# Optimization experiments

Hardware: AMD Instinct MI355X
Metric: run time of the kernel (lower is better)

Reference implementation:

```python
import jax, jax.numpy as jnp
import numpy as np
from jax import lax

B, C, H, W = 4, 256, 64, 64
M = 8
CP = C // M  # 32 attention channels
KS = (3, 5, 7, 9)
EPS = 1e-5


def conv1x1(a, w, b):
    # a: [B,Ci,H,W], w: [Co,Ci], b: [Co]
    return jnp.einsum('bchw,oc->bohw', a, w) + b[None, :, None, None]


def _patches(a, k):
    # im2col with padding k//2, stride 1 (matches torch.nn.Unfold(k,1,k//2,1))
    pad = k // 2
    p = lax.conv_general_dilated_patches(a, (k, k), (1, 1), [(pad, pad), (pad, pad)])
    Bb, Cc = a.shape[0], a.shape[1]
    return p.reshape(Bb, Cc, k * k, a.shape[2], a.shape[3])  # [B,C',k^2,H,W]


def local_attn(km, qm, xm, k):
    # query is the center of each patch == qm itself (stride 1, pad k//2)
    kp = _patches(km, k)                                   # [B,C',k^2,H,W]
    scores = jnp.einsum('bckhw,bchw->bkhw', kp, qm)        # per-pixel k^2 logits
    attn = jax.nn.softmax(scores, axis=1)                  # softmax over window (dim=-2 in torch)
    xp = _patches(xm, k)                                   # [B,C',k^2,H,W]
    return jnp.einsum('bckhw,bkhw->bchw', xp, attn)        # [B,C',H,W]


def setup_inputs() -> dict:
    key = jax.random.key(0)
    ks = jax.random.split(key, 12)
    s_in = 1.0 / np.sqrt(C)
    s_out = 1.0 / np.sqrt(CP)
    return {
        'x': jax.random.normal(ks[0], (B, C, H, W), jnp.float32),
        'vessel': jax.random.uniform(ks[1], (B, 1, H, W), jnp.float32),
        'wk': jax.random.normal(ks[2], (CP, C), jnp.float32) * s_in,
        'bk': jnp.zeros((CP,), jnp.float32),
        'wq': jax.random.normal(ks[3], (CP, C), jnp.float32) * s_in,
        'bq': jnp.zeros((CP,), jnp.float32),
        'wx': jax.random.normal(ks[4], (CP, C), jnp.float32) * s_in,
        'bx': jnp.zeros((CP,), jnp.float32),
        'wf': jax.random.normal(ks[5], (C, CP), jnp.float32) * s_out,
        'bf': jnp.zeros((C,), jnp.float32),
        'gamma': jnp.ones((C,), jnp.float32),
        'beta': jnp.zeros((C,), jnp.float32),
    }


def reference(x, vessel, wk, bk, wq, bq, wx, bx, wf, bf, gamma, beta):
    km = conv1x1(x, wk, bk) * vessel   # key map masked by vessel
    qm = conv1x1(x, wq, bq)            # query map
    xm = conv1x1(x, wx, bx)            # value map
    pre = local_attn(km, qm, xm, KS[0])
    for k in KS[1:]:
        pre = pre + local_attn(km, qm, xm, k)
    y = conv1x1(pre, wf, bf)           # [B,C,H,W]
    # BatchNorm2d (training-mode batch stats)
    mean = y.mean(axis=(0, 2, 3), keepdims=True)
    var = y.var(axis=(0, 2, 3), keepdims=True)
    yn = (y - mean) * lax.rsqrt(var + EPS)
    return x + gamma[None, :, None, None] * yn + beta[None, :, None, None]
```

## Files before the change

### kernel.cpp

```cpp
#include <hip/hip_runtime.h>
#include <hip/hip_bf16.h>

typedef __hip_bfloat16 bf16;
typedef unsigned short u16;
typedef unsigned int u32;

typedef __bf16 bf16x8 __attribute__((ext_vector_type(8)));
typedef float f32x4 __attribute__((ext_vector_type(4)));

__device__ __forceinline__ float bf2f(bf16 v) { return __bfloat162float(v); }
__device__ __forceinline__ float us2f(u16 u) {
    union { u32 i; float f; } c; c.i = ((u32)u) << 16; return c.f;
}
__device__ __forceinline__ u16 f2u(float f) {
    union { bf16 b; u16 u; } c; c.b = __float2bfloat16(f); return c.u;
}

__global__ __launch_bounds__(256) void k_proj(
    const float* __restrict__ x, const float* __restrict__ vessel,
    const float* __restrict__ wk, const float* __restrict__ bk,
    const float* __restrict__ wq, const float* __restrict__ bq,
    const float* __restrict__ wx, const float* __restrict__ bx,
    bf16* __restrict__ km, bf16* __restrict__ qm, bf16* __restrict__ xm,
    float* __restrict__ partials)
{
    __shared__ u16 xs[64 * 264];
    __shared__ u16 wsh[48 * 264];
    const int tid = threadIdx.x;
    const int bid = blockIdx.x;
    const int nh = bid & 1;
    const int pt = bid >> 1;
    const int b  = pt >> 6;
    const int p0 = (pt & 63) * 64;

    if (bid < 64) {
#pragma unroll
        for (int i = 0; i < 5; ++i) {
            const int idx = tid + i * 256;
            if (idx < 1056) partials[bid * 1056 + idx] = 0.f;
        }
    }

#pragma unroll
    for (int i = 0; i < 16; ++i) {
        const int idx4 = tid + i * 256;
        const int ch = idx4 >> 4;
        const int px4 = (idx4 & 15) * 4;
        const float4 v = *(const float4*)&x[(b * 256 + ch) * 4096 + p0 + px4];
        xs[(px4 + 0) * 264 + ch] = f2u(v.x);
        xs[(px4 + 1) * 264 + ch] = f2u(v.y);
        xs[(px4 + 2) * 264 + ch] = f2u(v.z);
        xs[(px4 + 3) * 264 + ch] = f2u(v.w);
    }
#pragma unroll
    for (int i = 0; i < 12; ++i) {
        const int idx4 = tid + i * 256;
        const int o = idx4 >> 6;
        const int ch4 = (idx4 & 63) * 4;
        const int go = nh * 48 + o;
        const float* wp = (go < 32) ? wk : ((go < 64) ? wq : wx);
        const float4 v = *(const float4*)&wp[(go & 31) * 256 + ch4];
        wsh[o * 264 + ch4 + 0] = f2u(v.x);
        wsh[o * 264 + ch4 + 1] = f2u(v.y);
        wsh[o * 264 + ch4 + 2] = f2u(v.z);
        wsh[o * 264 + ch4 + 3] = f2u(v.w);
    }
    __syncthreads();

    const int w = tid >> 6;
    const int lane = tid & 63;
    const int lm = lane & 15, quad = lane >> 4;

    f32x4 acc0 = {0.f, 0.f, 0.f, 0.f};
    f32x4 acc1 = {0.f, 0.f, 0.f, 0.f};
    f32x4 acc2 = {0.f, 0.f, 0.f, 0.f};
#pragma unroll
    for (int kk = 0; kk < 8; ++kk) {
        const int k0 = kk * 32 + quad * 8;
        const bf16x8 a  = *(const bf16x8*)&xs[(w * 16 + lm) * 264 + k0];
        const bf16x8 b0 = *(const bf16x8*)&wsh[(0 + lm) * 264 + k0];
        const bf16x8 b1 = *(const bf16x8*)&wsh[(16 + lm) * 264 + k0];
        const bf16x8 b2 = *(const bf16x8*)&wsh[(32 + lm) * 264 + k0];
        acc0 = __builtin_amdgcn_mfma_f32_16x16x32_bf16(a, b0, acc0, 0, 0, 0);
        acc1 = __builtin_amdgcn_mfma_f32_16x16x32_bf16(a, b1, acc1, 0, 0, 0);
        acc2 = __builtin_amdgcn_mfma_f32_16x16x32_bf16(a, b2, acc2, 0, 0, 0);
    }
#pragma unroll
    for (int t = 0; t < 3; ++t) {
        const f32x4 acc = (t == 0) ? acc0 : ((t == 1) ? acc1 : acc2);
        const int go = nh * 48 + t * 16 + lm;
        const float* bs = (go < 32) ? bk : ((go < 64) ? bq : bx);
        const float bias = bs[go & 31];
        bf16* dst = (go < 32) ? km : ((go < 64) ? qm : xm);
#pragma unroll
        for (int rg = 0; rg < 4; ++rg) {
            const int px = p0 + w * 16 + quad * 4 + rg;
            float vv = acc[rg] + bias;
            if (go < 32) vv *= vessel[b * 4096 + px];
            dst[(b * 4096 + px) * 32 + (go & 31)] = __float2bfloat16(vv);
        }
    }
}

__global__ __launch_bounds__(256, 3) void k_attn(
    const bf16* __restrict__ km, const bf16* __restrict__ qm,
    const bf16* __restrict__ xm, bf16* __restrict__ pre,
    float* __restrict__ partials)
{
    __shared__ u16 kT[192 * 40];
    __shared__ u16 xTt[32 * 200];
    __shared__ float S[32 * 196];
    u16* P = kT;
    u16* preT = (u16*)S;

    const int tid = threadIdx.x;
    const int b = blockIdx.x >> 7;
    const int t128 = blockIdx.x & 127;
    const int h0 = (t128 >> 3) * 4;
    const int w0 = (t128 & 7) * 8;
    const u16* uk = (const u16*)km;
    const u16* ux = (const u16*)xm;
    const u16* uq = (const u16*)qm;
    const uint4 z4 = {0u, 0u, 0u, 0u};

#pragma unroll
    for (int i = 0; i < 3; ++i) {
        const int idx4 = tid + i * 256;
        const int pos = idx4 >> 2, c8 = idx4 & 3;
        const int gh = h0 - 4 + (pos >> 4), gw = w0 - 4 + (pos & 15);
        uint4 kv = z4, xv = z4;
        if (gh >= 0 && gh < 64 && gw >= 0 && gw < 64) {
            const int g = ((b << 12) + (gh << 6) + gw) * 32 + c8 * 8;
            kv = *(const uint4*)&uk[g];
            xv = *(const uint4*)&ux[g];
        }
        *(uint4*)&kT[pos * 40 + c8 * 8] = kv;
        const u16* xu = (const u16*)&xv;
#pragma unroll
        for (int t = 0; t < 8; ++t)
            xTt[(c8 * 8 + t) * 200 + pos] = xu[t];
    }
    __syncthreads();

    const int w = tid >> 6;
    const int lane = tid & 63;
    const int lm = lane & 15, quad = lane >> 4;

#pragma unroll
    for (int i = 0; i < 6; ++i) {
        const int t = w + i * 4;
        const int m = t / 12, n = t - m * 12;
        const int am = m * 16 + lm;
        const int qgh = h0 + (am >> 3), qgw = w0 + (am & 7);
        const bf16x8 a =
            *(const bf16x8*)&uq[(((b << 12) + (qgh << 6) + qgw) << 5) + quad * 8];
        const bf16x8 bb = *(const bf16x8*)&kT[(n * 16 + lm) * 40 + quad * 8];
        f32x4 acc = {0.f, 0.f, 0.f, 0.f};
        acc = __builtin_amdgcn_mfma_f32_16x16x32_bf16(a, bb, acc, 0, 0, 0);
#pragma unroll
        for (int rg = 0; rg < 4; ++rg)
            S[(m * 16 + quad * 4 + rg) * 196 + n * 16 + lm] = acc[rg];
    }
    __syncthreads();

    const int px = tid >> 3, cg = tid & 7;
    const int ty = px >> 3, tx = px & 7;
    float e[24];
    float Z3 = 0.f, Z5 = 0.f, Z7 = 0.f, Z9 = 0.f;
#pragma unroll
    for (int i = 0; i < 24; ++i) {
        const int pos = cg + 8 * i;
        const int hy = pos >> 4, hx = pos & 15;
        const int dy = hy - 4 - ty, dx = hx - 4 - tx;
        const int ady = dy < 0 ? -dy : dy, adx = dx < 0 ? -dx : dx;
        const int r = ady > adx ? ady : adx;
        const float s = S[px * 196 + pos];
        const float ev = (r <= 4) ? __expf(s) : 0.f;
        e[i] = ev;
        if (r <= 1) Z3 += ev;
        if (r <= 2) Z5 += ev;
        if (r <= 3) Z7 += ev;
        Z9 += ev;
    }
#pragma unroll
    for (int m = 1; m <= 4; m <<= 1) {
        Z3 += __shfl_xor(Z3, m);
        Z5 += __shfl_xor(Z5, m);
        Z7 += __shfl_xor(Z7, m);
        Z9 += __shfl_xor(Z9, m);
    }
    const float iZ3 = 1.f / Z3, iZ5 = 1.f / Z5, iZ7 = 1.f / Z7, iZ9 = 1.f / Z9;
#pragma unroll
    for (int i = 0; i < 24; ++i) {
        const int pos = cg + 8 * i;
        const int hy = pos >> 4, hx = pos & 15;
        const int dy = hy - 4 - ty, dx = hx - 4 - tx;
        const int ady = dy < 0 ? -dy : dy, adx = dx < 0 ? -dx : dx;
        const int r = ady > adx ? ady : adx;
        float coef = iZ9;
        if (r <= 1) coef += iZ3;
        if (r <= 2) coef += iZ5;
        if (r <= 3) coef += iZ7;
        P[px * 200 + pos] = f2u(e[i] * coef);
    }
    __syncthreads();

    const int m0 = w >> 1, n0 = w & 1;
    f32x4 acc = {0.f, 0.f, 0.f, 0.f};
#pragma unroll
    for (int kk = 0; kk < 6; ++kk) {
        const int k0 = kk * 32 + quad * 8;
        const bf16x8 a = *(const bf16x8*)&P[(m0 * 16 + lm) * 200 + k0];
        const bf16x8 bb = *(const bf16x8*)&xTt[(n0 * 16 + lm) * 200 + k0];
        acc = __builtin_amdgcn_mfma_f32_16x16x32_bf16(a, bb, acc, 0, 0, 0);
    }
#pragma unroll
    for (int rg = 0; rg < 4; ++rg) {
        const int pl = m0 * 16 + quad * 4 + rg;
        const int gh = h0 + (pl >> 3), gw = w0 + (pl & 7);
        pre[(((b << 12) + (gh << 6) + gw) << 5) + n0 * 16 + lm] =
            __float2bfloat16(acc[rg]);
        preT[(n0 * 16 + lm) * 40 + pl] = f2u(acc[rg]);
    }
    __syncthreads();

    const int it = w >> 1, jt = w & 1;
    const bf16x8 ca = *(const bf16x8*)&preT[(it * 16 + lm) * 40 + quad * 8];
    const bf16x8 cb = *(const bf16x8*)&preT[(jt * 16 + lm) * 40 + quad * 8];
    f32x4 cacc = {0.f, 0.f, 0.f, 0.f};
    cacc = __builtin_amdgcn_mfma_f32_16x16x32_bf16(ca, cb, cacc, 0, 0, 0);
    float* pslot = &partials[(blockIdx.x & 63) * 1056];
#pragma unroll
    for (int rg = 0; rg < 4; ++rg) {
        const int ii = it * 16 + quad * 4 + rg, jj = jt * 16 + lm;
        atomicAdd(&pslot[ii * 32 + jj], cacc[rg]);
    }
    if (tid < 128) {
        const int cc = tid >> 2, sg = tid & 3;
        float s = 0.f;
#pragma unroll
        for (int p = 0; p < 8; ++p) s += us2f(preT[cc * 40 + sg * 8 + p]);
        s += __shfl_xor(s, 1);
        s += __shfl_xor(s, 2);
        if (sg == 0) atomicAdd(&pslot[1024 + cc], s);
    }
}

__global__ __launch_bounds__(256) void k_stats(
    const float* __restrict__ partials, const float* __restrict__ wf,
    const float* __restrict__ gamma, const float* __restrict__ beta,
    float* __restrict__ Aout, float* __restrict__ Sout,
    u16* __restrict__ wfh, u16* __restrict__ wfl)
{
    __shared__ float cov[1024];
    __shared__ float mu[32];
    const int tid = threadIdx.x;
    float4 a = {0.f, 0.f, 0.f, 0.f};
    for (int blk = 0; blk < 64; ++blk) {
        const float4 p = *(const float4*)&partials[blk * 1056 + tid * 4];
        a.x += p.x; a.y += p.y; a.z += p.z; a.w += p.w;
    }
    *(float4*)&cov[tid * 4] = a;
    if (tid < 32) {
        float s = 0.f;
        for (int blk = 0; blk < 64; ++blk) s += partials[blk * 1056 + 1024 + tid];
        mu[tid] = s * (1.f / 16384.f);
    }
    __syncthreads();
    float wo[32];
#pragma unroll
    for (int c = 0; c < 32; ++c) wo[c] = wf[tid * 32 + c];

    __attribute__((aligned(16))) u16 hb[32];
    __attribute__((aligned(16))) u16 lb[32];
#pragma unroll
    for (int c = 0; c < 32; ++c) {
        const float v = wo[c];
        const u16 h = f2u(v);
        hb[c] = h;
        lb[c] = f2u(v - us2f(h));
    }
#pragma unroll
    for (int c8 = 0; c8 < 4; ++c8) {
        *(uint4*)&wfh[tid * 32 + c8 * 8] = *(const uint4*)&hb[c8 * 8];
        *(uint4*)&wfl[tid * 32 + c8 * 8] = *(const uint4*)&lb[c8 * 8];
    }

    float mv = 0.f;
#pragma unroll
    for (int c = 0; c < 32; ++c) mv += wo[c] * mu[c];
    float qacc = 0.f;
    for (int i2 = 0; i2 < 32; ++i2) {
        float t = 0.f;
#pragma unroll
        for (int j2 = 0; j2 < 32; ++j2) t += wo[j2] * cov[i2 * 32 + j2];
        qacc += wo[i2] * t;
    }
    const float var = qacc * (1.f / 16384.f) - mv * mv;
    const float A = gamma[tid] * rsqrtf(var + 1e-5f);
    Aout[tid] = A;
    Sout[tid] = beta[tid] - A * mv;
}

__global__ __launch_bounds__(256) void k_out(
    const bf16* __restrict__ pre, const u16* __restrict__ wfh,
    const u16* __restrict__ wfl, const float* __restrict__ x,
    const float* __restrict__ A, const float* __restrict__ S,
    float* __restrict__ out)
{
    __shared__ u16 wh[256 * 40];
    __shared__ u16 wl[256 * 40];
    __shared__ u16 pL[32 * 40];
    const int tid = threadIdx.x;
    const int gp0 = blockIdx.x * 32;
    const int b = gp0 >> 12, p0 = gp0 & 4095;

#pragma unroll
    for (int i = 0; i < 4; ++i) {
        const int idx = tid + i * 256;
        const int o = idx >> 2, c8 = idx & 3;
        *(uint4*)&wh[o * 40 + c8 * 8] = *(const uint4*)&wfh[o * 32 + c8 * 8];
        *(uint4*)&wl[o * 40 + c8 * 8] = *(const uint4*)&wfl[o * 32 + c8 * 8];
    }
    if (tid < 128) {
        const int px = tid >> 2, c8 = tid & 3;
        *(uint4*)&pL[px * 40 + c8 * 8] =
            *(const uint4*)&((const u16*)pre)[(gp0 + px) * 32 + c8 * 8];
    }
    __syncthreads();

    const int w = tid >> 6;
    const int lane = tid & 63;
    const int lm = lane & 15, quad = lane >> 4;

    bf16x8 pb[2];
    pb[0] = *(const bf16x8*)&pL[(0 + lm) * 40 + quad * 8];
    pb[1] = *(const bf16x8*)&pL[(16 + lm) * 40 + quad * 8];

    f32x4 acc[4][2];
#pragma unroll
    for (int mm = 0; mm < 4; ++mm) {
        const int orow = w * 64 + mm * 16 + lm;
        const bf16x8 ah = *(const bf16x8*)&wh[orow * 40 + quad * 8];
        const bf16x8 al = *(const bf16x8*)&wl[orow * 40 + quad * 8];
#pragma unroll
        for (int n = 0; n < 2; ++n) {
            f32x4 t = {0.f, 0.f, 0.f, 0.f};
            t = __builtin_amdgcn_mfma_f32_16x16x32_bf16(ah, pb[n], t, 0, 0, 0);
            acc[mm][n] =
                __builtin_amdgcn_mfma_f32_16x16x32_bf16(al, pb[n], t, 0, 0, 0);
        }
    }

#pragma unroll
    for (int mm = 0; mm < 4; ++mm) {
#pragma unroll
        for (int rg = 0; rg < 4; ++rg) {
            const int o = w * 64 + mm * 16 + quad * 4 + rg;
            const float Ao = A[o], So = S[o];
#pragma unroll
            for (int n = 0; n < 2; ++n) {
                const int ga = ((b << 8) + o) * 4096 + p0 + n * 16 + lm;
                out[ga] = x[ga] + Ao * acc[mm][n][rg] + So;
            }
        }
    }
}

extern "C" void kernel_launch(void* const* d_in, const int* in_sizes, int n_in,
                              void* d_out, int out_size, void* d_ws, size_t ws_size,
                              hipStream_t stream)
{
    (void)in_sizes; (void)n_in; (void)out_size; (void)ws_size;
    float* out = (float*)d_out;
    char* ws = (char*)d_ws;

    const float* x      = (const float*)d_in[0];
    const float* vessel = (const float*)d_in[1];
    const float* wk     = (const float*)d_in[2];
    const float* bk     = (const float*)d_in[3];
    const float* wq     = (const float*)d_in[4];
    const float* bq     = (const float*)d_in[5];
    const float* wx     = (const float*)d_in[6];
    const float* bx     = (const float*)d_in[7];
    const float* wf     = (const float*)d_in[8];
    const float* gamma  = (const float*)d_in[10];
    const float* beta   = (const float*)d_in[11];

    bf16* km  = (bf16*)(ws);
    bf16* qm  = (bf16*)(ws + 1048576);
    bf16* xm  = (bf16*)(ws + 2097152);
    bf16* pre = (bf16*)(ws + 3145728);
    float* partials = (float*)(ws + 4194304);
    float* Abuf     = (float*)(ws + 4464640);
    float* Sbuf     = (float*)(ws + 4465664);
    u16*   wfh      = (u16*)  (ws + 4466688);
    u16*   wfl      = (u16*)  (ws + 4483072);

    k_proj <<<512, 256, 0, stream>>>(x, vessel, wk, bk, wq, bq, wx, bx,
                                     km, qm, xm, partials);
    k_attn <<<512, 256, 0, stream>>>(km, qm, xm, pre, partials);
    k_stats<<<  1, 256, 0, stream>>>(partials, wf, gamma, beta, Abuf, Sbuf,
                                     wfh, wfl);
    k_out  <<<512, 256, 0, stream>>>(pre, wfh, wfl, x, Abuf, Sbuf, out);
}
```

Before: 124.7 us.

## Shrink attention tiles to 4x4 and fold stats kernel into last block

The attention tile shrinks from 4x8 to 4x4 pixels with a 12x12 halo, doubling the grid to 1024 blocks and raising the occupancy target to 4 blocks per CU. LDS shrinks, and the padded K dimension is zeroed explicitly. The separate single-block stats kernel is removed: the last k_attn block, detected with an atomic counter, reduces the partials and computes the BN scale and shift. This saves a kernel launch and the serial gap, but the smaller tile loads proportionally more halo data, and the last-block reduction sits on the critical path.

```diff
diff --git a/kernel.cpp b/kernel.cpp
--- a/kernel.cpp
+++ b/kernel.cpp
@@ -22,7 +22,7 @@
     const float* __restrict__ wq, const float* __restrict__ bq,
     const float* __restrict__ wx, const float* __restrict__ bx,
     bf16* __restrict__ km, bf16* __restrict__ qm, bf16* __restrict__ xm,
-    float* __restrict__ partials)
+    float* __restrict__ partials, unsigned int* __restrict__ counter)
 {
     __shared__ u16 xs[64 * 264];
     __shared__ u16 wsh[48 * 264];
@@ -39,6 +39,7 @@
             const int idx = tid + i * 256;
             if (idx < 1056) partials[bid * 1056 + idx] = 0.f;
         }
+        if (bid == 0 && tid == 0) counter[0] = 0u;
     }
 
 #pragma unroll
@@ -102,22 +103,27 @@
     }
 }
 
-__global__ __launch_bounds__(256, 3) void k_attn(
+__global__ __launch_bounds__(256, 4) void k_attn(
     const bf16* __restrict__ km, const bf16* __restrict__ qm,
     const bf16* __restrict__ xm, bf16* __restrict__ pre,
-    float* __restrict__ partials)
+    float* __restrict__ partials, unsigned int* __restrict__ counter,
+    const float* __restrict__ wf, const float* __restrict__ gamma,
+    const float* __restrict__ beta,
+    float* __restrict__ Aout, float* __restrict__ Sout,
+    u16* __restrict__ wfh, u16* __restrict__ wfl)
 {
-    __shared__ u16 kT[192 * 40];
-    __shared__ u16 xTt[32 * 200];
-    __shared__ float S[32 * 196];
+    __shared__ u16 kT[144 * 40];
+    __shared__ u16 xTt[32 * 168];
+    __shared__ float S[16 * 148];
+    __shared__ int lastFlag;
     u16* P = kT;
     u16* preT = (u16*)S;
 
     const int tid = threadIdx.x;
-    const int b = blockIdx.x >> 7;
-    const int t128 = blockIdx.x & 127;
-    const int h0 = (t128 >> 3) * 4;
-    const int w0 = (t128 & 7) * 8;
+    const int b = blockIdx.x >> 8;
+    const int t256 = blockIdx.x & 255;
+    const int h0 = (t256 >> 4) * 4;
+    const int w0 = (t256 & 15) * 4;
     const u16* uk = (const u16*)km;
     const u16* ux = (const u16*)xm;
     const u16* uq = (const u16*)qm;
@@ -126,19 +132,28 @@
 #pragma unroll
     for (int i = 0; i < 3; ++i) {
         const int idx4 = tid + i * 256;
-        const int pos = idx4 >> 2, c8 = idx4 & 3;
-        const int gh = h0 - 4 + (pos >> 4), gw = w0 - 4 + (pos & 15);
-        uint4 kv = z4, xv = z4;
-        if (gh >= 0 && gh < 64 && gw >= 0 && gw < 64) {
-            const int g = ((b << 12) + (gh << 6) + gw) * 32 + c8 * 8;
-            kv = *(const uint4*)&uk[g];
-            xv = *(const uint4*)&ux[g];
-        }
-        *(uint4*)&kT[pos * 40 + c8 * 8] = kv;
-        const u16* xu = (const u16*)&xv;
-#pragma unroll
-        for (int t = 0; t < 8; ++t)
-            xTt[(c8 * 8 + t) * 200 + pos] = xu[t];
+        if (idx4 < 576) {
+            const int pos = idx4 >> 2, c8 = idx4 & 3;
+            const int hy = (pos * 683) >> 13, hx = pos - hy * 12;
+            const int gh = h0 - 4 + hy, gw = w0 - 4 + hx;
+            uint4 kv = z4, xv = z4;
+            if (gh >= 0 && gh < 64 && gw >= 0 && gw < 64) {
+                const int g = ((b << 12) + (gh << 6) + gw) * 32 + c8 * 8;
+                kv = *(const uint4*)&uk[g];
+                xv = *(const uint4*)&ux[g];
+            }
+            *(uint4*)&kT[pos * 40 + c8 * 8] = kv;
+            const u16* xu = (const u16*)&xv;
+#pragma unroll
+            for (int t = 0; t < 8; ++t)
+                xTt[(c8 * 8 + t) * 168 + pos] = xu[t];
+        }
+    }
+#pragma unroll
+    for (int i = 0; i < 2; ++i) {
+        const int id = tid + i * 256;
+        const int ch = id >> 4, j = id & 15;
+        if (j < 12) ((u32*)xTt)[ch * 84 + 72 + j] = 0u;
     }
     __syncthreads();
 
@@ -146,35 +161,33 @@
     const int lane = tid & 63;
     const int lm = lane & 15, quad = lane >> 4;
 
-#pragma unroll
-    for (int i = 0; i < 6; ++i) {
-        const int t = w + i * 4;
-        const int m = t / 12, n = t - m * 12;
-        const int am = m * 16 + lm;
-        const int qgh = h0 + (am >> 3), qgw = w0 + (am & 7);
+    {
+        const int qgh = h0 + (lm >> 2), qgw = w0 + (lm & 3);
         const bf16x8 a =
             *(const bf16x8*)&uq[(((b << 12) + (qgh << 6) + qgw) << 5) + quad * 8];
-        const bf16x8 bb = *(const bf16x8*)&kT[(n * 16 + lm) * 40 + quad * 8];
-        f32x4 acc = {0.f, 0.f, 0.f, 0.f};
-        acc = __builtin_amdgcn_mfma_f32_16x16x32_bf16(a, bb, acc, 0, 0, 0);
-#pragma unroll
-        for (int rg = 0; rg < 4; ++rg)
-            S[(m * 16 + quad * 4 + rg) * 196 + n * 16 + lm] = acc[rg];
-    }
-    __syncthreads();
-
-    const int px = tid >> 3, cg = tid & 7;
-    const int ty = px >> 3, tx = px & 7;
-    float e[24];
+        for (int n = w; n < 9; n += 4) {
+            const bf16x8 bb = *(const bf16x8*)&kT[(n * 16 + lm) * 40 + quad * 8];
+            f32x4 acc = {0.f, 0.f, 0.f, 0.f};
+            acc = __builtin_amdgcn_mfma_f32_16x16x32_bf16(a, bb, acc, 0, 0, 0);
+#pragma unroll
+            for (int rg = 0; rg < 4; ++rg)
+                S[(quad * 4 + rg) * 148 + n * 16 + lm] = acc[rg];
+        }
+    }
+    __syncthreads();
+
+    const int px = tid >> 4, cg = tid & 15;
+    const int ty = px >> 2, tx = px & 3;
+    float e[9];
     float Z3 = 0.f, Z5 = 0.f, Z7 = 0.f, Z9 = 0.f;
 #pragma unroll
-    for (int i = 0; i < 24; ++i) {
-        const int pos = cg + 8 * i;
-        const int hy = pos >> 4, hx = pos & 15;
+    for (int i = 0; i < 9; ++i) {
+        const int pos = cg + 16 * i;
+        const int hy = (pos * 683) >> 13, hx = pos - hy * 12;
         const int dy = hy - 4 - ty, dx = hx - 4 - tx;
         const int ady = dy < 0 ? -dy : dy, adx = dx < 0 ? -dx : dx;
         const int r = ady > adx ? ady : adx;
-        const float s = S[px * 196 + pos];
+        const float s = S[px * 148 + pos];
         const float ev = (r <= 4) ? __expf(s) : 0.f;
         e[i] = ev;
         if (r <= 1) Z3 += ev;
@@ -183,7 +196,7 @@
         Z9 += ev;
     }
 #pragma unroll
-    for (int m = 1; m <= 4; m <<= 1) {
+    for (int m = 1; m <= 8; m <<= 1) {
         Z3 += __shfl_xor(Z3, m);
         Z5 += __shfl_xor(Z5, m);
         Z7 += __shfl_xor(Z7, m);
@@ -191,9 +204,9 @@
     }
     const float iZ3 = 1.f / Z3, iZ5 = 1.f / Z5, iZ7 = 1.f / Z7, iZ9 = 1.f / Z9;
 #pragma unroll
-    for (int i = 0; i < 24; ++i) {
-        const int pos = cg + 8 * i;
-        const int hy = pos >> 4, hx = pos & 15;
+    for (int i = 0; i < 9; ++i) {
+        const int pos = cg + 16 * i;
+        const int hy = (pos * 683) >> 13, hx = pos - hy * 12;
         const int dy = hy - 4 - ty, dx = hx - 4 - tx;
         const int ady = dy < 0 ? -dy : dy, adx = dx < 0 ? -dx : dx;
         const int r = ady > adx ? ady : adx;
@@ -201,26 +214,33 @@
         if (r <= 1) coef += iZ3;
         if (r <= 2) coef += iZ5;
         if (r <= 3) coef += iZ7;
-        P[px * 200 + pos] = f2u(e[i] * coef);
-    }
-    __syncthreads();
-
-    const int m0 = w >> 1, n0 = w & 1;
-    f32x4 acc = {0.f, 0.f, 0.f, 0.f};
-#pragma unroll
-    for (int kk = 0; kk < 6; ++kk) {
-        const int k0 = kk * 32 + quad * 8;
-        const bf16x8 a = *(const bf16x8*)&P[(m0 * 16 + lm) * 200 + k0];
-        const bf16x8 bb = *(const bf16x8*)&xTt[(n0 * 16 + lm) * 200 + k0];
-        acc = __builtin_amdgcn_mfma_f32_16x16x32_bf16(a, bb, acc, 0, 0, 0);
-    }
-#pragma unroll
-    for (int rg = 0; rg < 4; ++rg) {
-        const int pl = m0 * 16 + quad * 4 + rg;
-        const int gh = h0 + (pl >> 3), gw = w0 + (pl & 7);
-        pre[(((b << 12) + (gh << 6) + gw) << 5) + n0 * 16 + lm] =
-            __float2bfloat16(acc[rg]);
-        preT[(n0 * 16 + lm) * 40 + pl] = f2u(acc[rg]);
+        P[px * 168 + pos] = f2u(e[i] * coef);
+    }
+    if (cg < 12) ((u32*)P)[px * 84 + 72 + cg] = 0u;
+    __syncthreads();
+
+    {
+        const int ch = tid >> 3, j = tid & 7;
+        ((u32*)preT)[ch * 20 + 8 + j] = 0u;
+    }
+    if (w < 2) {
+        const int n0 = w;
+        f32x4 acc = {0.f, 0.f, 0.f, 0.f};
+#pragma unroll
+        for (int kk = 0; kk < 5; ++kk) {
+            const int k0 = kk * 32 + quad * 8;
+            const bf16x8 a = *(const bf16x8*)&P[lm * 168 + k0];
+            const bf16x8 bb = *(const bf16x8*)&xTt[(n0 * 16 + lm) * 168 + k0];
+            acc = __builtin_amdgcn_mfma_f32_16x16x32_bf16(a, bb, acc, 0, 0, 0);
+        }
+#pragma unroll
+        for (int rg = 0; rg < 4; ++rg) {
+            const int pl = quad * 4 + rg;
+            const int gh = h0 + (pl >> 2), gw = w0 + (pl & 3);
+            pre[(((b << 12) + (gh << 6) + gw) << 5) + n0 * 16 + lm] =
+                __float2bfloat16(acc[rg]);
+            preT[(n0 * 16 + lm) * 40 + pl] = f2u(acc[rg]);
+        }
     }
     __syncthreads();
 
@@ -239,67 +259,73 @@
         const int cc = tid >> 2, sg = tid & 3;
         float s = 0.f;
 #pragma unroll
-        for (int p = 0; p < 8; ++p) s += us2f(preT[cc * 40 + sg * 8 + p]);
+        for (int p = 0; p < 4; ++p) s += us2f(preT[cc * 40 + sg * 4 + p]);
         s += __shfl_xor(s, 1);
         s += __shfl_xor(s, 2);
         if (sg == 0) atomicAdd(&pslot[1024 + cc], s);
     }
-}
-
-__global__ __launch_bounds__(256) void k_stats(
-    const float* __restrict__ partials, const float* __restrict__ wf,
-    const float* __restrict__ gamma, const float* __restrict__ beta,
-    float* __restrict__ Aout, float* __restrict__ Sout,
-    u16* __restrict__ wfh, u16* __restrict__ wfl)
-{
-    __shared__ float cov[1024];
-    __shared__ float mu[32];
-    const int tid = threadIdx.x;
-    float4 a = {0.f, 0.f, 0.f, 0.f};
-    for (int blk = 0; blk < 64; ++blk) {
-        const float4 p = *(const float4*)&partials[blk * 1056 + tid * 4];
-        a.x += p.x; a.y += p.y; a.z += p.z; a.w += p.w;
-    }
-    *(float4*)&cov[tid * 4] = a;
-    if (tid < 32) {
-        float s = 0.f;
-        for (int blk = 0; blk < 64; ++blk) s += partials[blk * 1056 + 1024 + tid];
-        mu[tid] = s * (1.f / 16384.f);
-    }
-    __syncthreads();
-    float wo[32];
-#pragma unroll
-    for (int c = 0; c < 32; ++c) wo[c] = wf[tid * 32 + c];
-
-    __attribute__((aligned(16))) u16 hb[32];
-    __attribute__((aligned(16))) u16 lb[32];
-#pragma unroll
-    for (int c = 0; c < 32; ++c) {
-        const float v = wo[c];
-        const u16 h = f2u(v);
-        hb[c] = h;
-        lb[c] = f2u(v - us2f(h));
-    }
-#pragma unroll
-    for (int c8 = 0; c8 < 4; ++c8) {
-        *(uint4*)&wfh[tid * 32 + c8 * 8] = *(const uint4*)&hb[c8 * 8];
-        *(uint4*)&wfl[tid * 32 + c8 * 8] = *(const uint4*)&lb[c8 * 8];
-    }
-
-    float mv = 0.f;
-#pragma unroll
-    for (int c = 0; c < 32; ++c) mv += wo[c] * mu[c];
-    float qacc = 0.f;
-    for (int i2 = 0; i2 < 32; ++i2) {
-        float t = 0.f;
-#pragma unroll
-        for (int j2 = 0; j2 < 32; ++j2) t += wo[j2] * cov[i2 * 32 + j2];
-        qacc += wo[i2] * t;
-    }
-    const float var = qacc * (1.f / 16384.f) - mv * mv;
-    const float A = gamma[tid] * rsqrtf(var + 1e-5f);
-    Aout[tid] = A;
-    Sout[tid] = beta[tid] - A * mv;
+
+    __syncthreads();
+    if (tid == 0) {
+        __threadfence();
+        const unsigned int old = atomicAdd(counter, 1u);
+        lastFlag = (old == 1023u) ? 1 : 0;
+    }
+    __syncthreads();
+    if (lastFlag) {
+        float* cov = (float*)kT;
+        float* mu  = cov + 1024;
+        float4 a4 = {0.f, 0.f, 0.f, 0.f};
+        for (int blk = 0; blk < 64; ++blk) {
+            const float* pp = &partials[blk * 1056 + tid * 4];
+            a4.x += __hip_atomic_load(&pp[0], __ATOMIC_RELAXED, __HIP_MEMORY_SCOPE_AGENT);
+            a4.y += __hip_atomic_load(&pp[1], __ATOMIC_RELAXED, __HIP_MEMORY_SCOPE_AGENT);
+            a4.z += __hip_atomic_load(&pp[2], __ATOMIC_RELAXED, __HIP_MEMORY_SCOPE_AGENT);
+            a4.w += __hip_atomic_load(&pp[3], __ATOMIC_RELAXED, __HIP_MEMORY_SCOPE_AGENT);
+        }
+        *(float4*)&cov[tid * 4] = a4;
+        if (tid < 32) {
+            float s = 0.f;
+            for (int blk = 0; blk < 64; ++blk)
+                s += __hip_atomic_load(&partials[blk * 1056 + 1024 + tid],
+                                       __ATOMIC_RELAXED, __HIP_MEMORY_SCOPE_AGENT);
+            mu[tid] = s * (1.f / 16384.f);
+        }
+        __syncthreads();
+        float wo[32];
+#pragma unroll
+        for (int c = 0; c < 32; ++c) wo[c] = wf[tid * 32 + c];
+
+        __attribute__((aligned(16))) u16 hb[32];
+        __attribute__((aligned(16))) u16 lb[32];
+#pragma unroll
+        for (int c = 0; c < 32; ++c) {
+            const float v = wo[c];
+            const u16 h = f2u(v);
+            hb[c] = h;
+            lb[c] = f2u(v - us2f(h));
+        }
+#pragma unroll
+        for (int c8 = 0; c8 < 4; ++c8) {
+            *(uint4*)&wfh[tid * 32 + c8 * 8] = *(const uint4*)&hb[c8 * 8];
+            *(uint4*)&wfl[tid * 32 + c8 * 8] = *(const uint4*)&lb[c8 * 8];
+        }
+
+        float mv = 0.f;
+#pragma unroll
+        for (int c = 0; c < 32; ++c) mv += wo[c] * mu[c];
+        float qacc = 0.f;
+        for (int i2 = 0; i2 < 32; ++i2) {
+            float tt = 0.f;
+#pragma unroll
+            for (int j2 = 0; j2 < 32; ++j2) tt += wo[j2] * cov[i2 * 32 + j2];
+            qacc += wo[i2] * tt;
+        }
+        const float var = qacc * (1.f / 16384.f) - mv * mv;
+        const float A = gamma[tid] * rsqrtf(var + 1e-5f);
+        Aout[tid] = A;
+        Sout[tid] = beta[tid] - A * mv;
+    }
 }
 
 __global__ __launch_bounds__(256) void k_out(
@@ -391,16 +417,16 @@
     bf16* qm  = (bf16*)(ws + 1048576);
     bf16* xm  = (bf16*)(ws + 2097152);
     bf16* pre = (bf16*)(ws + 3145728);
-    float* partials = (float*)(ws + 4194304);
-    float* Abuf     = (float*)(ws + 4464640);
-    float* Sbuf     = (float*)(ws + 4465664);
-    u16*   wfh      = (u16*)  (ws + 4466688);
-    u16*   wfl      = (u16*)  (ws + 4483072);
-
-    k_proj <<<512, 256, 0, stream>>>(x, vessel, wk, bk, wq, bq, wx, bx,
-                                     km, qm, xm, partials);
-    k_attn <<<512, 256, 0, stream>>>(km, qm, xm, pre, partials);
-    k_stats<<<  1, 256, 0, stream>>>(partials, wf, gamma, beta, Abuf, Sbuf,
-                                     wfh, wfl);
-    k_out  <<<512, 256, 0, stream>>>(pre, wfh, wfl, x, Abuf, Sbuf, out);
-}
+    float* partials       = (float*)(ws + 4194304);
+    unsigned int* counter = (unsigned int*)(ws + 4464640);
+    float* Abuf = (float*)(ws + 4465664);
+    float* Sbuf = (float*)(ws + 4466688);
+    u16*   wfh  = (u16*)  (ws + 4467712);
+    u16*   wfl  = (u16*)  (ws + 4484096);
+
+    k_proj <<< 512, 256, 0, stream>>>(x, vessel, wk, bk, wq, bq, wx, bx,
+                                      km, qm, xm, partials, counter);
+    k_attn <<<1024, 256, 0, stream>>>(km, qm, xm, pre, partials, counter,
+                                      wf, gamma, beta, Abuf, Sbuf, wfh, wfl);
+    k_out  <<< 512, 256, 0, stream>>>(pre, wfh, wfl, x, Abuf, Sbuf, out);
+}
```

New measurement: 157.3 us. +26.1%, slower.
